# Performance work log

Hardware: AMD Instinct MI355X
Metric: run time of the kernel (lower is better)

The kernel has to match this reference:

```python
import jax, jax.numpy as jnp
import numpy as np

B, C, H, W = 4, 256, 64, 64
RC = 32  # reduced channels = C // reduction


def setup_inputs() -> dict:
    key = jax.random.key(0)
    ks = jax.random.split(key, 5)
    return {
        "x": jax.random.normal(ks[0], (B, C, H, W), dtype=jnp.float32),
        "context": jax.random.normal(ks[1], (B, C, H, W), dtype=jnp.float32),
        "Wq": jax.random.normal(ks[2], (RC, C), dtype=jnp.float32) * 0.02,
        "bq": jnp.zeros((RC,), dtype=jnp.float32),
        "Wk": jax.random.normal(ks[3], (RC, C), dtype=jnp.float32) * 0.02,
        "bk": jnp.zeros((RC,), dtype=jnp.float32),
        "Wv": jax.random.normal(ks[4], (C, C), dtype=jnp.float32) * 0.02,
        "bv": jnp.zeros((C,), dtype=jnp.float32),
        "gamma": jnp.ones((1,), dtype=jnp.float32),
    }


def reference(x, context, Wq, bq, Wk, bk, Wv, bv, gamma):
    b, c, h, w = x.shape
    _, _, hc, wc = context.shape
    n, m = h * w, hc * wc
    xf = x.reshape(b, c, n)          # (B,C,N)
    cf = context.reshape(b, c, m)    # (B,C,M)
    # 1x1 conv projections == per-pixel linear
    q = jnp.einsum('rc,bcn->bnr', Wq, xf) + bq            # (B,N,RC)
    k = jnp.einsum('rc,bcm->brm', Wk, cf) + bk[:, None]   # (B,RC,M)
    v = jnp.einsum('dc,bcm->bdm', Wv, cf) + bv[:, None]   # (B,C,M)
    scale = 1.0 / jnp.sqrt(jnp.asarray(q.shape[-1], dtype=q.dtype))
    attn = jax.nn.softmax(jnp.einsum('bnr,brm->bnm', q, k) * scale, axis=-1)  # (B,N,M)
    out = jnp.einsum('bdm,bnm->bdn', v, attn).reshape(b, c, h, w)
    return gamma * out + x
```

## Files before the change

kernel.cpp:

```cpp
#include <hip/hip_runtime.h>
#include <hip/hip_bf16.h>


#define B_ 4
#define C_ 256
#define N_ 4096
#define M_ 4096
#define SCALE_ 0.17677669529663687f

typedef __bf16 bf16x8 __attribute__((ext_vector_type(8)));
typedef float f32x4 __attribute__((ext_vector_type(4)));
typedef float f32x16 __attribute__((ext_vector_type(16)));
typedef int i32x8 __attribute__((ext_vector_type(8)));

#define AS1 __attribute__((address_space(1)))
#define AS3 __attribute__((address_space(3)))

static __device__ __forceinline__ unsigned short f2bf(float f) {
    unsigned int u = __float_as_uint(f);
    return (unsigned short)((u + 0x7fffu + ((u >> 16) & 1u)) >> 16);
}
static __device__ __forceinline__ unsigned bfpk(float a, float b) {
    return (unsigned)f2bf(a) | ((unsigned)f2bf(b) << 16);
}
static __device__ __forceinline__ void p_barrier() {
    asm volatile("s_waitcnt lgkmcnt(0)" ::: "memory");
    __builtin_amdgcn_s_barrier();
    asm volatile("" ::: "memory");
}

__global__ __launch_bounds__(256) void prep(
        const float* __restrict__ Wq, const float* __restrict__ Wk,
        const float* __restrict__ Wv, uint4* __restrict__ Wqf,
        uint4* __restrict__ Wkf, uint4* __restrict__ Wvf) {
    int bid = blockIdx.x, t = threadIdx.x;
    const float* W;
    uint4* dst;
    int frag;
    if (bid < 32)      { W = Wv; dst = Wvf; frag = (bid * 256 + t) >> 6; }
    else if (bid < 36) { W = Wq; dst = Wqf; frag = ((bid - 32) * 256 + t) >> 6; }
    else               { W = Wk; dst = Wkf; frag = ((bid - 36) * 256 + t) >> 6; }
    int lane = t & 63, low = lane & 15, q = lane >> 4;
    int fch = frag & 7, fr = frag >> 3;
    const float* wp = W + (size_t)(fr * 16 + low) * C_ + fch * 32 + q * 8;
    float4 w0 = *(const float4*)wp;
    float4 w1 = *(const float4*)(wp + 4);
    uint4 pk = {bfpk(w0.x, w0.y), bfpk(w0.z, w0.w),
                bfpk(w1.x, w1.y), bfpk(w1.z, w1.w)};
    dst[(size_t)frag * 64 + lane] = pk;
}

__global__ __launch_bounds__(256, 2) void fused_proj(
        const float* __restrict__ x, const float* __restrict__ ctx,
        const uint4* __restrict__ Wqf, const uint4* __restrict__ Wkf,
        const uint4* __restrict__ Wvf,
        const float* __restrict__ bq, const float* __restrict__ bk,
        const float* __restrict__ bv,
        unsigned short* __restrict__ Qf, unsigned short* __restrict__ Kf,
        unsigned char* __restrict__ Vf) {
    __shared__ unsigned short X[64][264];
    __shared__ unsigned short Pl[4][16 * 40];
    __shared__ unsigned char  Vw[4][16 * 40];

    int bid = blockIdx.x;
    bool isX = bid >= 256;
    int lb = bid & 255;
    int b = lb >> 6, pt64 = lb & 63;
    const float* __restrict__ in = (isX ? x : ctx) + (size_t)b * C_ * N_ + pt64 * 64;
    int t = threadIdx.x, wg = t >> 6, lane = t & 63;
    int low = lane & 15, q = lane >> 4;

    {
        int pL = lane;
        const float* s0 = in + pL;
#pragma unroll
        for (int ct = 0; ct < 4; ct++) {
            const float* s2 = s0 + (size_t)(ct * 64 + wg * 16) * N_;
            float v[16];
#pragma unroll
            for (int k = 0; k < 16; k++) v[k] = s2[(size_t)k * N_];
#pragma unroll
            for (int k = 0; k < 16; k += 2)
                *(unsigned*)&X[pL][ct * 64 + wg * 16 + k] = bfpk(v[k], v[k + 1]);
        }
    }
    __syncthreads();

    {
        const uint4* __restrict__ Wf = isX ? Wqf : Wkf;
        const float* __restrict__ bias = isX ? bq : bk;
        unsigned short* __restrict__ dst = isX ? Qf : Kf;
        bf16x8 xf[8];
#pragma unroll
        for (int ch = 0; ch < 8; ch++)
            xf[ch] = *(const bf16x8*)&X[wg * 16 + low][ch * 32 + q * 8];
        const f32x4 zero = {0.f, 0.f, 0.f, 0.f};
        f32x4 acc[2] = {zero, zero};
#pragma unroll
        for (int rt = 0; rt < 2; rt++)
#pragma unroll
            for (int ch = 0; ch < 8; ch++) {
                uint4 wv = Wf[(rt * 8 + ch) * 64 + lane];
                acc[rt] = __builtin_amdgcn_mfma_f32_16x16x32_bf16(
                    __builtin_bit_cast(bf16x8, wv), xf[ch], acc[rt], 0, 0, 0);
            }
        unsigned short* Pw = &Pl[wg][0];
#pragma unroll
        for (int rt = 0; rt < 2; rt++) {
            float b0 = bias[rt * 16 + q * 4 + 0], b1 = bias[rt * 16 + q * 4 + 1];
            float b2 = bias[rt * 16 + q * 4 + 2], b3 = bias[rt * 16 + q * 4 + 3];
            uint2 pk = {bfpk(acc[rt][0] + b0, acc[rt][1] + b1),
                        bfpk(acc[rt][2] + b2, acc[rt][3] + b3)};
            *(uint2*)(Pw + low * 40 + rt * 16 + q * 4) = pk;
        }
        uint4 frag = *(const uint4*)(Pw + low * 40 + q * 8);
        ((uint4*)dst)[((size_t)b * 256 + pt64 * 4 + wg) * 64 + lane] = frag;
    }

    if (!isX) {
        int mstep = wg >> 1, dh = wg & 1;
        bf16x8 vfr[2][8];
#pragma unroll
        for (int mt = 0; mt < 2; mt++)
#pragma unroll
            for (int ch = 0; ch < 8; ch++)
                vfr[mt][ch] = *(const bf16x8*)&X[mstep * 32 + mt * 16 + low][ch * 32 + q * 8];
        unsigned char* Vv = &Vw[wg][0];
        int msg = pt64 * 2 + mstep;
        const f32x4 zero = {0.f, 0.f, 0.f, 0.f};
#pragma unroll
        for (int dt8 = 0; dt8 < 8; dt8++) {
            int dt = dh * 8 + dt8;
            f32x4 a0 = zero, a1 = zero;
#pragma unroll
            for (int ch = 0; ch < 8; ch++) {
                uint4 wv = Wvf[(dt * 8 + ch) * 64 + lane];
                bf16x8 wfr = __builtin_bit_cast(bf16x8, wv);
                a0 = __builtin_amdgcn_mfma_f32_16x16x32_bf16(vfr[0][ch], wfr, a0, 0, 0, 0);
                a1 = __builtin_amdgcn_mfma_f32_16x16x32_bf16(vfr[1][ch], wfr, a1, 0, 0, 0);
            }
            float bb = bv[dt * 16 + low];
            unsigned w0 = __builtin_amdgcn_cvt_pk_fp8_f32(a0[0] + bb, a0[1] + bb, 0, false);
            w0 = __builtin_amdgcn_cvt_pk_fp8_f32(a0[2] + bb, a0[3] + bb, w0, true);
            unsigned w1 = __builtin_amdgcn_cvt_pk_fp8_f32(a1[0] + bb, a1[1] + bb, 0, false);
            w1 = __builtin_amdgcn_cvt_pk_fp8_f32(a1[2] + bb, a1[3] + bb, w1, true);
            *(unsigned*)(Vv + low * 40 + q * 4) = w0;
            *(unsigned*)(Vv + low * 40 + 16 + q * 4) = w1;
            uint2 fr = *(const uint2*)(Vv + low * 40 + q * 8);
            ((uint2*)Vf)[(((size_t)b * 128 + msg) * 16 + dt) * 64 + lane] = fr;
        }
    }
}

__global__ __launch_bounds__(512, 4) void attn(
        const unsigned short* __restrict__ Qf, const unsigned short* __restrict__ Kf,
        const unsigned char* __restrict__ Vf, const float* __restrict__ x,
        const float* __restrict__ gamma, float* __restrict__ out) {
    __shared__ __align__(16) unsigned char Pb[2][2][2 * 16 * 80];
    __shared__ float l_sh[4][32];
    __shared__ unsigned Obuf[32 * 129];
    __shared__ unsigned Ot[32 * 129];

    int bid = blockIdx.x;
    int xcd = bid & 7;
    int b = xcd >> 1;
    int ng = ((xcd & 1) << 6) | (bid >> 3);

    int wave = threadIdx.x >> 6, lane = threadIdx.x & 63;
    int g = wave >> 2, wg = wave & 3;
    int q = lane >> 4, low = lane & 15;
    int hi = lane >> 5;
    int dsel = q & 1;
    int l31 = lane & 31;
    int t = wg & 1;
    int h = wg >> 1;

    const uint4* Qp = (const uint4*)Qf;
    const uint4* Kp = (const uint4*)Kf + (size_t)b * 256 * 64;
    const uint2* Vq = (const uint2*)(Vf + (size_t)b * 1048576) + (size_t)hi * 1024 + low;
    int slab0 = g * 32;

    bf16x8 qa = __builtin_bit_cast(bf16x8, Qp[(size_t)(b * 256 + ng * 2 + t) * 64 + lane]);

    f32x16 acc2[2];
    acc2[0] = (f32x16)(0.f);
    acc2[1] = (f32x16)(0.f);
    float lacc = 0.f;
    const f32x4 zero = {0.f, 0.f, 0.f, 0.f};

    unsigned char* PbG = &Pb[g][0][0];

    uint4 kv[2];
    f32x4 s[2];
    {
#pragma unroll
        for (int u = 0; u < 2; u++)
            kv[u] = Kp[(size_t)(slab0 * 4 + h * 2 + u) * 64 + lane];
#pragma unroll
        for (int u = 0; u < 2; u++)
            s[u] = __builtin_amdgcn_mfma_f32_16x16x32_bf16(
                __builtin_bit_cast(bf16x8, kv[u]), qa, zero, 0, 0, 0);
#pragma unroll
        for (int u = 0; u < 2; u++)
            kv[u] = Kp[(size_t)((slab0 + 1) * 4 + h * 2 + u) * 64 + lane];
        unsigned char* Pw = PbG;
#pragma unroll
        for (int u = 0; u < 2; u++) {
            float p0 = __expf(s[u][0] * SCALE_), p1 = __expf(s[u][1] * SCALE_);
            float p2 = __expf(s[u][2] * SCALE_), p3 = __expf(s[u][3] * SCALE_);
            lacc += p0 + p1 + p2 + p3;
            unsigned w = __builtin_amdgcn_cvt_pk_fp8_f32(p0, p1, 0, false);
            w = __builtin_amdgcn_cvt_pk_fp8_f32(p2, p3, w, true);
            *(unsigned*)(Pw + t * 1280 + low * 80 + h * 32 + u * 16 + q * 4) = w;
        }
    }
    i32x8 vf[2];
#pragma unroll
    for (int dg = 0; dg < 2; dg++) {
        int dt = wg * 4 + dg * 2 + dsel;
        const uint2* Vs = Vq + (size_t)slab0 * 2048 + dt * 64;
        long* dqw = (long*)&vf[dg];
#pragma unroll
        for (int ss = 0; ss < 4; ss++)
            dqw[ss] = *(const long*)(Vs + ss * 16);
    }
    p_barrier();

    for (int i = 0; i < 32; i++) {
        int cur = i & 1, nxt = cur ^ 1;
        bool hn = (i + 1 < 32);

        if (hn) {
#pragma unroll
            for (int u = 0; u < 2; u++)
                s[u] = __builtin_amdgcn_mfma_f32_16x16x32_bf16(
                    __builtin_bit_cast(bf16x8, kv[u]), qa, zero, 0, 0, 0);
            if (i + 2 < 32) {
#pragma unroll
                for (int u = 0; u < 2; u++)
                    kv[u] = Kp[(size_t)((slab0 + i + 2) * 4 + h * 2 + u) * 64 + lane];
            }
        }

        {
            const unsigned char* pr = PbG + cur * 2560 + dsel * 1280 + low * 80 + hi * 32;
            i32x8 pf;
            ((uint4*)&pf)[0] = *(const uint4*)pr;
            ((uint4*)&pf)[1] = *(const uint4*)(pr + 16);
#pragma unroll
            for (int dg = 0; dg < 2; dg++)
                acc2[dg] = __builtin_amdgcn_mfma_scale_f32_32x32x64_f8f6f4(
                    vf[dg], pf, acc2[dg], 0, 0, 0, 127, 0, 127);
        }

        if (hn) {
#pragma unroll
            for (int dg = 0; dg < 2; dg++) {
                int dt = wg * 4 + dg * 2 + dsel;
                const uint2* Vs = Vq + (size_t)(slab0 + i + 1) * 2048 + dt * 64;
                long* dqw = (long*)&vf[dg];
#pragma unroll
                for (int ss = 0; ss < 4; ss++)
                    dqw[ss] = *(const long*)(Vs + ss * 16);
            }
        }

        if (hn) {
            unsigned char* Pw = PbG + nxt * 2560;
#pragma unroll
            for (int u = 0; u < 2; u++) {
                float p0 = __expf(s[u][0] * SCALE_), p1 = __expf(s[u][1] * SCALE_);
                float p2 = __expf(s[u][2] * SCALE_), p3 = __expf(s[u][3] * SCALE_);
                lacc += p0 + p1 + p2 + p3;
                unsigned w = __builtin_amdgcn_cvt_pk_fp8_f32(p0, p1, 0, false);
                w = __builtin_amdgcn_cvt_pk_fp8_f32(p2, p3, w, true);
                *(unsigned*)(Pw + t * 1280 + low * 80 + h * 32 + u * 16 + q * 4) = w;
            }
        }
        p_barrier();
    }

    lacc += __shfl_xor(lacc, 16, 64);
    lacc += __shfl_xor(lacc, 32, 64);
    if (lane < 16)
        l_sh[g * 2 + h][t * 16 + low] = lacc;

    if (g == 1) {
#pragma unroll
        for (int dg = 0; dg < 2; dg++)
#pragma unroll
            for (int k = 0; k < 8; k++) {
                int col16 = wg * 32 + dg * 16 + (k & 1) + 4 * (k >> 1) + 2 * hi;
                Obuf[l31 * 129 + col16] = bfpk(acc2[dg][2 * k], acc2[dg][2 * k + 1]);
            }
    }
    __syncthreads();
    if (g == 0) {
#pragma unroll
        for (int dg = 0; dg < 2; dg++)
#pragma unroll
            for (int k = 0; k < 8; k++) {
                int col16 = wg * 32 + dg * 16 + (k & 1) + 4 * (k >> 1) + 2 * hi;
                unsigned pk = Obuf[l31 * 129 + col16];
                float a = acc2[dg][2 * k]     + __uint_as_float(pk << 16);
                float c = acc2[dg][2 * k + 1] + __uint_as_float(pk & 0xffff0000u);
                Ot[l31 * 129 + col16] = bfpk(a, c);
            }
    }
    __syncthreads();

    {
        float gm = gamma[0];
        float rinv = gm / (l_sh[0][l31] + l_sh[1][l31] + l_sh[2][l31] + l_sh[3][l31]);
        int dh = hi;
        size_t nb = ((size_t)(b * 256 + wave * 32 + dh * 16)) * 4096
                    + (size_t)ng * 32 + l31;
#pragma unroll 4
        for (int j = 0; j < 16; j++) {
            unsigned pk = Ot[l31 * 129 + wave * 16 + dh * 8 + (j >> 1)];
            unsigned bits = (j & 1) ? (pk & 0xffff0000u) : (pk << 16);
            float o = __uint_as_float(bits);
            size_t idx = nb + (size_t)j * 4096;
            out[idx] = o * rinv + x[idx];
        }
    }
}

extern "C" void kernel_launch(void* const* d_in, const int* in_sizes, int n_in,
                              void* d_out, int out_size, void* d_ws, size_t ws_size,
                              hipStream_t stream) {
    const float* x     = (const float*)d_in[0];
    const float* ctx   = (const float*)d_in[1];
    const float* Wq    = (const float*)d_in[2];
    const float* bq    = (const float*)d_in[3];
    const float* Wk    = (const float*)d_in[4];
    const float* bk    = (const float*)d_in[5];
    const float* Wv    = (const float*)d_in[6];
    const float* bv    = (const float*)d_in[7];
    const float* gamma = (const float*)d_in[8];
    float* out = (float*)d_out;

    unsigned short* Qf = (unsigned short*)d_ws;
    unsigned short* Kf = Qf + (size_t)B_ * N_ * 32;
    unsigned char*  Vf = (unsigned char*)(Kf + (size_t)B_ * M_ * 32);
    uint4* Wqf = (uint4*)(Vf + (size_t)B_ * M_ * C_);
    uint4* Wkf = Wqf + 16 * 64;
    uint4* Wvf = Wkf + 16 * 64;

    prep<<<40, 256, 0, stream>>>(Wq, Wk, Wv, Wqf, Wkf, Wvf);
    fused_proj<<<512, 256, 0, stream>>>(x, ctx, Wqf, Wkf, Wvf, bq, bk, bv, Qf, Kf, Vf);
    attn<<<512, 512, 0, stream>>>(Qf, Kf, Vf, x, gamma, out);
}
```

Before: 144.3 us.

## Drop split-M wave groups in attention; use exp2 with prescaled log2e

The attention block shrinks from 512 to 256 threads. Each wave now walks all 64 key slabs instead of two wave groups splitting M in half and merging partial outputs through shared memory, so the Obuf reduction, one barrier and the extra LDS go away. The serial loop per wave doubles, and each CU has half as many threads in flight to hide latency. Softmax exponentials switch from __expf to the hardware exp2 with the scale folded together with log2(e).

```diff
diff --git a/kernel.cpp b/kernel.cpp
--- a/kernel.cpp
+++ b/kernel.cpp
@@ -6,7 +6,7 @@
 #define C_ 256
 #define N_ 4096
 #define M_ 4096
-#define SCALE_ 0.17677669529663687f
+#define SCALE2_ 0.25509558269734695f
 
 typedef __bf16 bf16x8 __attribute__((ext_vector_type(8)));
 typedef float f32x4 __attribute__((ext_vector_type(4)));
@@ -152,13 +152,12 @@
     }
 }
 
-__global__ __launch_bounds__(512, 4) void attn(
+__global__ __launch_bounds__(256, 4) void attn(
         const unsigned short* __restrict__ Qf, const unsigned short* __restrict__ Kf,
         const unsigned char* __restrict__ Vf, const float* __restrict__ x,
         const float* __restrict__ gamma, float* __restrict__ out) {
-    __shared__ __align__(16) unsigned char Pb[2][2][2 * 16 * 80];
-    __shared__ float l_sh[4][32];
-    __shared__ unsigned Obuf[32 * 129];
+    __shared__ __align__(16) unsigned char Pb[2][2560];
+    __shared__ float l_sh[2][32];
     __shared__ unsigned Ot[32 * 129];
 
     int bid = blockIdx.x;
@@ -166,8 +165,7 @@
     int b = xcd >> 1;
     int ng = ((xcd & 1) << 6) | (bid >> 3);
 
-    int wave = threadIdx.x >> 6, lane = threadIdx.x & 63;
-    int g = wave >> 2, wg = wave & 3;
+    int wg = threadIdx.x >> 6, lane = threadIdx.x & 63;
     int q = lane >> 4, low = lane & 15;
     int hi = lane >> 5;
     int dsel = q & 1;
@@ -178,7 +176,6 @@
     const uint4* Qp = (const uint4*)Qf;
     const uint4* Kp = (const uint4*)Kf + (size_t)b * 256 * 64;
     const uint2* Vq = (const uint2*)(Vf + (size_t)b * 1048576) + (size_t)hi * 1024 + low;
-    int slab0 = g * 32;
 
     bf16x8 qa = __builtin_bit_cast(bf16x8, Qp[(size_t)(b * 256 + ng * 2 + t) * 64 + lane]);
 
@@ -188,26 +185,26 @@
     float lacc = 0.f;
     const f32x4 zero = {0.f, 0.f, 0.f, 0.f};
 
-    unsigned char* PbG = &Pb[g][0][0];
-
     uint4 kv[2];
     f32x4 s[2];
     {
 #pragma unroll
         for (int u = 0; u < 2; u++)
-            kv[u] = Kp[(size_t)(slab0 * 4 + h * 2 + u) * 64 + lane];
+            kv[u] = Kp[(size_t)(h * 2 + u) * 64 + lane];
 #pragma unroll
         for (int u = 0; u < 2; u++)
             s[u] = __builtin_amdgcn_mfma_f32_16x16x32_bf16(
                 __builtin_bit_cast(bf16x8, kv[u]), qa, zero, 0, 0, 0);
 #pragma unroll
         for (int u = 0; u < 2; u++)
-            kv[u] = Kp[(size_t)((slab0 + 1) * 4 + h * 2 + u) * 64 + lane];
-        unsigned char* Pw = PbG;
+            kv[u] = Kp[(size_t)(4 + h * 2 + u) * 64 + lane];
+        unsigned char* Pw = &Pb[0][0];
 #pragma unroll
         for (int u = 0; u < 2; u++) {
-            float p0 = __expf(s[u][0] * SCALE_), p1 = __expf(s[u][1] * SCALE_);
-            float p2 = __expf(s[u][2] * SCALE_), p3 = __expf(s[u][3] * SCALE_);
+            float p0 = __builtin_amdgcn_exp2f(s[u][0] * SCALE2_);
+            float p1 = __builtin_amdgcn_exp2f(s[u][1] * SCALE2_);
+            float p2 = __builtin_amdgcn_exp2f(s[u][2] * SCALE2_);
+            float p3 = __builtin_amdgcn_exp2f(s[u][3] * SCALE2_);
             lacc += p0 + p1 + p2 + p3;
             unsigned w = __builtin_amdgcn_cvt_pk_fp8_f32(p0, p1, 0, false);
             w = __builtin_amdgcn_cvt_pk_fp8_f32(p2, p3, w, true);
@@ -218,7 +215,7 @@
 #pragma unroll
     for (int dg = 0; dg < 2; dg++) {
         int dt = wg * 4 + dg * 2 + dsel;
-        const uint2* Vs = Vq + (size_t)slab0 * 2048 + dt * 64;
+        const uint2* Vs = Vq + dt * 64;
         long* dqw = (long*)&vf[dg];
 #pragma unroll
         for (int ss = 0; ss < 4; ss++)
@@ -226,24 +223,24 @@
     }
     p_barrier();
 
-    for (int i = 0; i < 32; i++) {
+    for (int i = 0; i < 64; i++) {
         int cur = i & 1, nxt = cur ^ 1;
-        bool hn = (i + 1 < 32);
+        bool hn = (i + 1 < 64);
 
         if (hn) {
 #pragma unroll
             for (int u = 0; u < 2; u++)
                 s[u] = __builtin_amdgcn_mfma_f32_16x16x32_bf16(
                     __builtin_bit_cast(bf16x8, kv[u]), qa, zero, 0, 0, 0);
-            if (i + 2 < 32) {
+            if (i + 2 < 64) {
 #pragma unroll
                 for (int u = 0; u < 2; u++)
-                    kv[u] = Kp[(size_t)((slab0 + i + 2) * 4 + h * 2 + u) * 64 + lane];
+                    kv[u] = Kp[(size_t)((i + 2) * 4 + h * 2 + u) * 64 + lane];
             }
         }
 
         {
-            const unsigned char* pr = PbG + cur * 2560 + dsel * 1280 + low * 80 + hi * 32;
+            const unsigned char* pr = &Pb[cur][0] + dsel * 1280 + low * 80 + hi * 32;
             i32x8 pf;
             ((uint4*)&pf)[0] = *(const uint4*)pr;
             ((uint4*)&pf)[1] = *(const uint4*)(pr + 16);
@@ -257,7 +254,7 @@
 #pragma unroll
             for (int dg = 0; dg < 2; dg++) {
                 int dt = wg * 4 + dg * 2 + dsel;
-                const uint2* Vs = Vq + (size_t)(slab0 + i + 1) * 2048 + dt * 64;
+                const uint2* Vs = Vq + (size_t)(i + 1) * 2048 + dt * 64;
                 long* dqw = (long*)&vf[dg];
 #pragma unroll
                 for (int ss = 0; ss < 4; ss++)
@@ -266,11 +263,13 @@
         }
 
         if (hn) {
-            unsigned char* Pw = PbG + nxt * 2560;
+            unsigned char* Pw = &Pb[nxt][0];
 #pragma unroll
             for (int u = 0; u < 2; u++) {
-                float p0 = __expf(s[u][0] * SCALE_), p1 = __expf(s[u][1] * SCALE_);
-                float p2 = __expf(s[u][2] * SCALE_), p3 = __expf(s[u][3] * SCALE_);
+                float p0 = __builtin_amdgcn_exp2f(s[u][0] * SCALE2_);
+                float p1 = __builtin_amdgcn_exp2f(s[u][1] * SCALE2_);
+                float p2 = __builtin_amdgcn_exp2f(s[u][2] * SCALE2_);
+                float p3 = __builtin_amdgcn_exp2f(s[u][3] * SCALE2_);
                 lacc += p0 + p1 + p2 + p3;
                 unsigned w = __builtin_amdgcn_cvt_pk_fp8_f32(p0, p1, 0, false);
                 w = __builtin_amdgcn_cvt_pk_fp8_f32(p2, p3, w, true);
@@ -283,45 +282,33 @@
     lacc += __shfl_xor(lacc, 16, 64);
     lacc += __shfl_xor(lacc, 32, 64);
     if (lane < 16)
-        l_sh[g * 2 + h][t * 16 + low] = lacc;
-
-    if (g == 1) {
-#pragma unroll
-        for (int dg = 0; dg < 2; dg++)
-#pragma unroll
-            for (int k = 0; k < 8; k++) {
-                int col16 = wg * 32 + dg * 16 + (k & 1) + 4 * (k >> 1) + 2 * hi;
-                Obuf[l31 * 129 + col16] = bfpk(acc2[dg][2 * k], acc2[dg][2 * k + 1]);
-            }
-    }
-    __syncthreads();
-    if (g == 0) {
-#pragma unroll
-        for (int dg = 0; dg < 2; dg++)
-#pragma unroll
-            for (int k = 0; k < 8; k++) {
-                int col16 = wg * 32 + dg * 16 + (k & 1) + 4 * (k >> 1) + 2 * hi;
-                unsigned pk = Obuf[l31 * 129 + col16];
-                float a = acc2[dg][2 * k]     + __uint_as_float(pk << 16);
-                float c = acc2[dg][2 * k + 1] + __uint_as_float(pk & 0xffff0000u);
-                Ot[l31 * 129 + col16] = bfpk(a, c);
-            }
-    }
+        l_sh[h][t * 16 + low] = lacc;
+
+#pragma unroll
+    for (int dg = 0; dg < 2; dg++)
+#pragma unroll
+        for (int k = 0; k < 8; k++) {
+            int col16 = wg * 32 + dg * 16 + (k & 1) + 4 * (k >> 1) + 2 * hi;
+            Ot[l31 * 129 + col16] = bfpk(acc2[dg][2 * k], acc2[dg][2 * k + 1]);
+        }
     __syncthreads();
 
     {
         float gm = gamma[0];
-        float rinv = gm / (l_sh[0][l31] + l_sh[1][l31] + l_sh[2][l31] + l_sh[3][l31]);
+        float rinv = gm / (l_sh[0][l31] + l_sh[1][l31]);
         int dh = hi;
-        size_t nb = ((size_t)(b * 256 + wave * 32 + dh * 16)) * 4096
-                    + (size_t)ng * 32 + l31;
+#pragma unroll
+        for (int dq = 0; dq < 2; dq++) {
+            size_t nb = ((size_t)(b * 256 + wg * 64 + dq * 32 + dh * 16)) * 4096
+                        + (size_t)ng * 32 + l31;
 #pragma unroll 4
-        for (int j = 0; j < 16; j++) {
-            unsigned pk = Ot[l31 * 129 + wave * 16 + dh * 8 + (j >> 1)];
-            unsigned bits = (j & 1) ? (pk & 0xffff0000u) : (pk << 16);
-            float o = __uint_as_float(bits);
-            size_t idx = nb + (size_t)j * 4096;
-            out[idx] = o * rinv + x[idx];
+            for (int j = 0; j < 16; j++) {
+                unsigned pk = Ot[l31 * 129 + wg * 32 + dq * 16 + dh * 8 + (j >> 1)];
+                unsigned bits = (j & 1) ? (pk & 0xffff0000u) : (pk << 16);
+                float o = __uint_as_float(bits);
+                size_t idx = nb + (size_t)j * 4096;
+                out[idx] = o * rinv + x[idx];
+            }
         }
     }
 }
@@ -349,5 +336,5 @@
 
     prep<<<40, 256, 0, stream>>>(Wq, Wk, Wv, Wqf, Wkf, Wvf);
     fused_proj<<<512, 256, 0, stream>>>(x, ctx, Wqf, Wkf, Wvf, bq, bk, bv, Qf, Kf, Vf);
-    attn<<<512, 512, 0, stream>>>(Qf, Kf, Vf, x, gamma, out);
-}
+    attn<<<512, 256, 0, stream>>>(Qf, Kf, Vf, x, gamma, out);
+}
```

Result: no change. 145.0 us (+0.5%).
